# Performance work log

Hardware: AMD Instinct MI355X
Metric: run time of the kernel (lower is better)

The kernel has to match this reference:

```python
import jax, jax.numpy as jnp
import numpy as np

B, L, D = 16, 1024, 768   # batch, nodes per graph, embed_dim
H, C = 4, 256             # gat_heads, gat_hidden per head
E = 8192                  # directed edges per graph (2 per triple)
NEG_SLOPE = 0.2           # PyG GATConv default negative_slope


def setup_inputs() -> dict:
    key = jax.random.key(0)
    ks = jax.random.split(key, 8)
    s = 0.02
    return {
        "text_embeddings": jax.random.normal(ks[0], (B, L, D), jnp.float32),
        "edge_index": jax.random.randint(ks[1], (B, 2, E), 0, L, jnp.int32),
        "W_gat": jax.random.normal(ks[2], (H * C, D), jnp.float32) * s,   # GATConv.lin (bias=False)
        "att_src": jax.random.normal(ks[3], (H, C), jnp.float32) * s,
        "att_dst": jax.random.normal(ks[4], (H, C), jnp.float32) * s,
        "b_gat": jnp.zeros((H * C,), jnp.float32),                        # GATConv bias (concat=True)
        "W_out": jax.random.normal(ks[5], (D, H * C + D), jnp.float32) * s,
        "b_out": jnp.zeros((D,), jnp.float32),
    }


def _gat_one(x, edge_index, W_gat, att_src, att_dst, b_gat):
    """PyG-style GATConv on one graph. x: [N,D], edge_index: [2,E] (src->dst)."""
    N = x.shape[0]
    loops = jnp.arange(N, dtype=edge_index.dtype)          # add_self_loops=True (PyG default)
    src = jnp.concatenate([edge_index[0], loops])
    dst = jnp.concatenate([edge_index[1], loops])
    h = (x @ W_gat.T).reshape(N, H, C)                     # [N,H,C]
    a_s = jnp.einsum('nhc,hc->nh', h, att_src)             # [N,H]
    a_d = jnp.einsum('nhc,hc->nh', h, att_dst)
    e = jax.nn.leaky_relu(a_s[src] + a_d[dst], NEG_SLOPE)  # [E+N,H] per-edge logits
    m = jax.ops.segment_max(e, dst, num_segments=N)        # stable softmax over each dst neighborhood
    p = jnp.exp(e - m[dst])
    denom = jax.ops.segment_sum(p, dst, num_segments=N)
    alpha = p / (denom[dst] + 1e-16)                       # [E+N,H]
    out = jax.ops.segment_sum(alpha[:, :, None] * h[src], dst, num_segments=N)  # [N,H,C]
    return out.reshape(N, H * C) + b_gat


def reference(text_embeddings, edge_index, W_gat, att_src, att_dst, b_gat, W_out, b_out):
    x_gat = jax.vmap(_gat_one, in_axes=(0, 0, None, None, None, None))(
        text_embeddings, edge_index, W_gat, att_src, att_dst, b_gat)   # [B,L,H*C]
    fused = jnp.concatenate([text_embeddings, x_gat], axis=-1)          # [B,L,D+H*C]
    return fused @ W_out.T + b_out                                      # [B,L,D]
```

## Files before the change

### kernel.cpp

```cpp
#include <hip/hip_runtime.h>
#include <hip/hip_bf16.h>

#define B_ 16
#define L_ 1024
#define D_ 768
#define H_ 4
#define C_ 256
#define E_ 8192
#define ET_ (E_ + L_)
#define HC_ (H_ * C_)
#define F_ (D_ + HC_)
#define M_ (B_ * L_)
#define NEG_SLOPE 0.2f

typedef short bf16x8 __attribute__((ext_vector_type(8)));
typedef float f32x4 __attribute__((ext_vector_type(4)));
using bf16 = __hip_bfloat16;

struct bf16x4_s { bf16 x, y, z, w; };

__device__ __forceinline__ void async_copy16(const bf16* gsrc, bf16* ldst) {
  __builtin_amdgcn_global_load_lds(
      (const __attribute__((address_space(1))) unsigned int*)gsrc,
      (__attribute__((address_space(3))) unsigned int*)ldst, 16, 0, 0);
}

__global__ void cast_x_strided(const float* __restrict__ x, bf16* __restrict__ xf) {
  int idx = blockIdx.x * blockDim.x + threadIdx.x;
  if (idx >= M_ * (D_ / 8)) return;
  int row = idx / (D_ / 8);
  int c8 = idx - row * (D_ / 8);
  const float4* src = (const float4*)(x + (long)row * D_ + c8 * 8);
  float4 v0 = src[0], v1 = src[1];
  bf16 o[8];
  o[0] = __float2bfloat16(v0.x); o[1] = __float2bfloat16(v0.y);
  o[2] = __float2bfloat16(v0.z); o[3] = __float2bfloat16(v0.w);
  o[4] = __float2bfloat16(v1.x); o[5] = __float2bfloat16(v1.y);
  o[6] = __float2bfloat16(v1.z); o[7] = __float2bfloat16(v1.w);
  *(uint4*)(xf + (long)row * F_ + c8 * 8) = *(const uint4*)o;
}

__global__ void cast_two(const float4* __restrict__ a, bf16x4_s* __restrict__ oa, long na4,
                         const float4* __restrict__ bsrc, bf16x4_s* __restrict__ ob, long nb4) {
  long i = (long)blockIdx.x * blockDim.x + threadIdx.x;
  long stride = (long)gridDim.x * blockDim.x;
  for (; i < na4 + nb4; i += stride) {
    const float4 v = (i < na4) ? a[i] : bsrc[i - na4];
    bf16x4_s o;
    o.x = __float2bfloat16(v.x);
    o.y = __float2bfloat16(v.y);
    o.z = __float2bfloat16(v.z);
    o.w = __float2bfloat16(v.w);
    if (i < na4) oa[i] = o; else ob[i - na4] = o;
  }
}

#define BM 128
#define BN 128
#define BK 64

template <int OUT_BF16, int ATTN>
__global__ __launch_bounds__(256)
void gemm_nt_128(const bf16* __restrict__ A, int lda,
                 const bf16* __restrict__ Bm, int ldb,
                 void* __restrict__ Cm_, int ldc, int K,
                 const float* __restrict__ bias,
                 const float* __restrict__ att_s, const float* __restrict__ att_d,
                 float* __restrict__ a_sd)
{
  __shared__ __align__(16) bf16 As[BM * BK];
  __shared__ __align__(16) bf16 Bs[BN * BK];
  const int t = threadIdx.x;
  const int lane = t & 63;
  const int wave = t >> 6;
  const long m0 = (long)blockIdx.x * BM;
  const long n0 = (long)blockIdx.y * BN;
  const int wm = (wave >> 1) * 64;
  const int wn = (wave & 1) * 64;
  const int lrow = lane & 15;
  const int kq = lane >> 4;

  const int sr_base = wave * 32;
  const int sr_lane = lane >> 3;
  const int c8l = lane & 7;

  f32x4 acc[4][4] = {};

  for (int k0 = 0; k0 < K; k0 += BK) {
#pragma unroll
    for (int j = 0; j < 4; j++) {
      int r = sr_base + j * 8 + sr_lane;
      int col = k0 + ((c8l ^ (r & 7)) << 3);
      bf16* ldsA = As + (sr_base + j * 8) * BK;
      bf16* ldsB = Bs + (sr_base + j * 8) * BK;
      async_copy16(A + (m0 + r) * lda + col, ldsA);
      async_copy16(Bm + (n0 + r) * ldb + col, ldsB);
    }
    __syncthreads();
#pragma unroll
    for (int ks = 0; ks < BK; ks += 32) {
      bf16x8 af[4], bfr[4];
#pragma unroll
      for (int i = 0; i < 4; i++) {
        int ra = wm + i * 16 + lrow;
        int ca = ((ks >> 3) + kq) ^ (ra & 7);
        af[i] = *(const bf16x8*)(As + ra * BK + ca * 8);
        int rb = wn + i * 16 + lrow;
        int cb = ((ks >> 3) + kq) ^ (rb & 7);
        bfr[i] = *(const bf16x8*)(Bs + rb * BK + cb * 8);
      }
#pragma unroll
      for (int i = 0; i < 4; i++)
#pragma unroll
        for (int j = 0; j < 4; j++)
          acc[i][j] = __builtin_amdgcn_mfma_f32_16x16x32_bf16(af[i], bfr[j], acc[i][j], 0, 0, 0);
    }
    __syncthreads();
  }

#pragma unroll
  for (int i = 0; i < 4; i++) {
    long rbase = m0 + wm + i * 16 + (lane >> 4) * 4;
#pragma unroll
    for (int j = 0; j < 4; j++) {
      long col = n0 + wn + j * 16 + (lane & 15);
      float bv = bias ? bias[col] : 0.f;
#pragma unroll
      for (int r = 0; r < 4; r++) {
        long idx = (rbase + r) * ldc + col;
        float v = acc[i][j][r] + bv;
        if (OUT_BF16) ((bf16*)Cm_)[idx] = __float2bfloat16(v);
        else          ((float*)Cm_)[idx] = v;
      }
    }
  }

  if (ATTN) {
    float as_c[4], ad_c[4];
#pragma unroll
    for (int j = 0; j < 4; j++) {
      int col = (int)(n0 + wn + j * 16 + (lane & 15));
      as_c[j] = att_s[col];
      ad_c[j] = att_d[col];
    }
    const int head = (int)((n0 + wn) >> 8);
#pragma unroll
    for (int i = 0; i < 4; i++) {
#pragma unroll
      for (int r = 0; r < 4; r++) {
        float ps = 0.f, pd = 0.f;
#pragma unroll
        for (int j = 0; j < 4; j++) {
          float v = acc[i][j][r];
          ps += v * as_c[j];
          pd += v * ad_c[j];
        }
#pragma unroll
        for (int off = 1; off < 16; off <<= 1) {
          ps += __shfl_xor(ps, off);
          pd += __shfl_xor(pd, off);
        }
        if ((lane & 15) == 0) {
          long row = m0 + wm + i * 16 + (lane >> 4) * 4 + r;
          atomicAdd(a_sd + row * 8 + head, ps);
          atomicAdd(a_sd + row * 8 + 4 + head, pd);
        }
      }
    }
  }
}

__global__ void deg_count(const int* __restrict__ ei, int* __restrict__ deg) {
  int idx = blockIdx.x * blockDim.x + threadIdx.x;
  if (idx >= B_ * ET_) return;
  int b = idx / ET_, e = idx - b * ET_;
  int dst = (e < E_) ? ei[(long)b * 2 * E_ + E_ + e] : (e - E_);
  atomicAdd(&deg[b * L_ + dst], 1);
}

__global__ __launch_bounds__(1024)
void scan_offsets(const int* __restrict__ deg, int* __restrict__ offs,
                  int* __restrict__ cursor) {
  __shared__ int sh[1024];
  int b = blockIdx.x, t = threadIdx.x;
  int v = deg[b * L_ + t];
  sh[t] = v;
  __syncthreads();
  for (int d = 1; d < 1024; d <<= 1) {
    int x = (t >= d) ? sh[t - d] : 0;
    __syncthreads();
    sh[t] += x;
    __syncthreads();
  }
  int excl = sh[t] - v;
  offs[b * L_ + t] = excl;
  cursor[b * L_ + t] = excl;
}

__global__ void csr_fill(const int* __restrict__ ei, int* __restrict__ cursor,
                         int* __restrict__ csr_src) {
  int idx = blockIdx.x * blockDim.x + threadIdx.x;
  if (idx >= B_ * ET_) return;
  int b = idx / ET_, e = idx - b * ET_;
  int src, dst;
  if (e < E_) {
    src = ei[(long)b * 2 * E_ + e];
    dst = ei[(long)b * 2 * E_ + E_ + e];
  } else {
    src = dst = e - E_;
  }
  int slot = atomicAdd(&cursor[b * L_ + dst], 1);
  csr_src[(long)b * ET_ + slot] = src;
}

__device__ inline float lrelu(float v) { return v > 0.f ? v : NEG_SLOPE * v; }

__device__ __forceinline__ float sel4(float a0, float a1, float a2, float a3, int h) {
  float lo = (h & 1) ? a1 : a0;
  float hi = (h & 1) ? a3 : a2;
  return (h & 2) ? hi : lo;
}

__device__ __forceinline__ void fma8(float* acc, float a, uint4 u) {
#pragma unroll
  for (int k = 0; k < 4; k++) {
    unsigned w = ((const unsigned*)&u)[k];
    float lo = __uint_as_float(w << 16);
    float hi = __uint_as_float(w & 0xffff0000u);
    acc[2 * k]     += a * lo;
    acc[2 * k + 1] += a * hi;
  }
}

__global__ __launch_bounds__(256)
void gat_aggregate(const int* __restrict__ offs, const int* __restrict__ deg_a,
                   const int* __restrict__ csr_src,
                   const float* __restrict__ a_sd,
                   const bf16* __restrict__ h, bf16* __restrict__ xg, int ldx)
{
  const int bd = blockIdx.x * 4 + (threadIdx.x >> 6);
  const int b = bd >> 10;
  const int lane = threadIdx.x & 63;
  const int deg = deg_a[bd];
  const int* list = csr_src + (long)b * ET_ + offs[bd];
  const float4 ad = *(const float4*)(a_sd + (long)bd * 8 + 4);
  const int myhead = lane >> 4;
  const bf16* hbase = h + (long)b * L_ * HC_ + lane * 16;

  float acc16[16];
#pragma unroll
  for (int k = 0; k < 16; k++) acc16[k] = 0.f;

  if (deg <= 64) {
    int s_lane = 0;
    float4 e4 = {-INFINITY, -INFINITY, -INFINITY, -INFINITY};
    if (lane < deg) {
      s_lane = list[lane];
      const float4 as4 = *(const float4*)(a_sd + ((long)b * L_ + s_lane) * 8);
      e4.x = lrelu(as4.x + ad.x);
      e4.y = lrelu(as4.y + ad.y);
      e4.z = lrelu(as4.z + ad.z);
      e4.w = lrelu(as4.w + ad.w);
    }
    float4 mx = e4;
#pragma unroll
    for (int off = 32; off; off >>= 1) {
      mx.x = fmaxf(mx.x, __shfl_xor(mx.x, off));
      mx.y = fmaxf(mx.y, __shfl_xor(mx.y, off));
      mx.z = fmaxf(mx.z, __shfl_xor(mx.z, off));
      mx.w = fmaxf(mx.w, __shfl_xor(mx.w, off));
    }
    float4 p = {0.f, 0.f, 0.f, 0.f};
    if (lane < deg) {
      p.x = __expf(e4.x - mx.x);
      p.y = __expf(e4.y - mx.y);
      p.z = __expf(e4.z - mx.z);
      p.w = __expf(e4.w - mx.w);
    }
    float4 sm = p;
#pragma unroll
    for (int off = 32; off; off >>= 1) {
      sm.x += __shfl_xor(sm.x, off);
      sm.y += __shfl_xor(sm.y, off);
      sm.z += __shfl_xor(sm.z, off);
      sm.w += __shfl_xor(sm.w, off);
    }
    float4 alpha;
    alpha.x = p.x / (sm.x + 1e-16f);
    alpha.y = p.y / (sm.y + 1e-16f);
    alpha.z = p.z / (sm.z + 1e-16f);
    alpha.w = p.w / (sm.w + 1e-16f);

#pragma unroll 2
    for (int e = 0; e < deg; e++) {
      int se = __shfl(s_lane, e);
      float a0 = __shfl(alpha.x, e);
      float a1 = __shfl(alpha.y, e);
      float a2 = __shfl(alpha.z, e);
      float a3 = __shfl(alpha.w, e);
      float a = sel4(a0, a1, a2, a3, myhead);
      const bf16* hp = hbase + (long)se * HC_;
      uint4 u0 = *(const uint4*)hp;
      uint4 u1 = *(const uint4*)(hp + 8);
      fma8(acc16, a, u0);
      fma8(acc16 + 8, a, u1);
    }
  } else {
    float4 mx = {-INFINITY, -INFINITY, -INFINITY, -INFINITY};
    for (int i = lane; i < deg; i += 64) {
      int s = list[i];
      const float4 as4 = *(const float4*)(a_sd + ((long)b * L_ + s) * 8);
      mx.x = fmaxf(mx.x, lrelu(as4.x + ad.x));
      mx.y = fmaxf(mx.y, lrelu(as4.y + ad.y));
      mx.z = fmaxf(mx.z, lrelu(as4.z + ad.z));
      mx.w = fmaxf(mx.w, lrelu(as4.w + ad.w));
    }
#pragma unroll
    for (int off = 32; off; off >>= 1) {
      mx.x = fmaxf(mx.x, __shfl_xor(mx.x, off));
      mx.y = fmaxf(mx.y, __shfl_xor(mx.y, off));
      mx.z = fmaxf(mx.z, __shfl_xor(mx.z, off));
      mx.w = fmaxf(mx.w, __shfl_xor(mx.w, off));
    }
    float4 sm = {0.f, 0.f, 0.f, 0.f};
    for (int i = lane; i < deg; i += 64) {
      int s = list[i];
      const float4 as4 = *(const float4*)(a_sd + ((long)b * L_ + s) * 8);
      sm.x += __expf(lrelu(as4.x + ad.x) - mx.x);
      sm.y += __expf(lrelu(as4.y + ad.y) - mx.y);
      sm.z += __expf(lrelu(as4.z + ad.z) - mx.z);
      sm.w += __expf(lrelu(as4.w + ad.w) - mx.w);
    }
#pragma unroll
    for (int off = 32; off; off >>= 1) {
      sm.x += __shfl_xor(sm.x, off);
      sm.y += __shfl_xor(sm.y, off);
      sm.z += __shfl_xor(sm.z, off);
      sm.w += __shfl_xor(sm.w, off);
    }
    float4 rden;
    rden.x = 1.f / (sm.x + 1e-16f);
    rden.y = 1.f / (sm.y + 1e-16f);
    rden.z = 1.f / (sm.z + 1e-16f);
    rden.w = 1.f / (sm.w + 1e-16f);
    for (int e = 0; e < deg; e++) {
      int se = list[e];
      const float4 as4 = *(const float4*)(a_sd + ((long)b * L_ + se) * 8);
      float a0 = __expf(lrelu(as4.x + ad.x) - mx.x) * rden.x;
      float a1 = __expf(lrelu(as4.y + ad.y) - mx.y) * rden.y;
      float a2 = __expf(lrelu(as4.z + ad.z) - mx.z) * rden.z;
      float a3 = __expf(lrelu(as4.w + ad.w) - mx.w) * rden.w;
      float a = sel4(a0, a1, a2, a3, myhead);
      const bf16* hp = hbase + (long)se * HC_;
      uint4 u0 = *(const uint4*)hp;
      uint4 u1 = *(const uint4*)(hp + 8);
      fma8(acc16, a, u0);
      fma8(acc16 + 8, a, u1);
    }
  }

  bf16 ov[16];
#pragma unroll
  for (int k = 0; k < 16; k++) ov[k] = __float2bfloat16(acc16[k]);
  bf16* op = xg + (long)bd * ldx + lane * 16;
  *(uint4*)op = *(const uint4*)ov;
  *(uint4*)(op + 8) = *(const uint4*)(ov + 8);
}

__global__ void cout_kernel(const float* __restrict__ W_out, const float* __restrict__ b_gat,
                            const float* __restrict__ b_out, float* __restrict__ cout)
{
  int o = blockIdx.x * blockDim.x + threadIdx.x;
  if (o >= D_) return;
  float s = b_out[o];
  const float* wrow = W_out + (long)o * F_ + D_;
  for (int j = 0; j < HC_; j++) s += b_gat[j] * wrow[j];
  cout[o] = s;
}

extern "C" void kernel_launch(void* const* d_in, const int* in_sizes, int n_in,
                              void* d_out, int out_size, void* d_ws, size_t ws_size,
                              hipStream_t stream) {
  const float* x     = (const float*)d_in[0];
  const int*   ei    = (const int*)d_in[1];
  const float* Wg    = (const float*)d_in[2];
  const float* att_s = (const float*)d_in[3];
  const float* att_d = (const float*)d_in[4];
  const float* bgat  = (const float*)d_in[5];
  const float* Wout  = (const float*)d_in[6];
  const float* bout  = (const float*)d_in[7];
  float* out = (float*)d_out;

  char* ws = (char*)d_ws;
  size_t off = 0;
  auto alloc = [&](size_t bytes) {
    void* p = ws + off;
    off = (off + bytes + 255) & ~(size_t)255;
    return p;
  };
  bf16* xf      = (bf16*)alloc((size_t)M_ * F_ * 2);
  bf16* wg_bf   = (bf16*)alloc((size_t)HC_ * D_ * 2);
  bf16* wout_bf = (bf16*)alloc((size_t)D_ * F_ * 2);
  bf16* h_bf    = (bf16*)alloc((size_t)M_ * HC_ * 2);
  float* a_sd   = (float*)alloc((size_t)M_ * 8 * 4);
  int* deg      = (int*)alloc((size_t)M_ * 4);
  int* offs     = (int*)alloc((size_t)M_ * 4);
  int* cursor   = (int*)alloc((size_t)M_ * 4);
  int* csr_src  = (int*)alloc((size_t)B_ * ET_ * 4);
  float* cout   = (float*)alloc((size_t)D_ * 4);

  {
    int nchunk = M_ * (D_ / 8);
    cast_x_strided<<<dim3((nchunk + 255) / 256), dim3(256), 0, stream>>>(x, xf);
    long na4 = (long)HC_ * D_ / 4, nb4 = (long)D_ * F_ / 4;
    cast_two<<<dim3((int)((na4 + nb4 + 255) / 256)), dim3(256), 0, stream>>>(
        (const float4*)Wg, (bf16x4_s*)wg_bf, na4,
        (const float4*)Wout, (bf16x4_s*)wout_bf, nb4);
  }

  hipMemsetAsync(a_sd, 0, (size_t)M_ * 8 * 4 + (size_t)M_ * 4, stream);
  {
    int nedge = B_ * ET_;
    deg_count<<<dim3((nedge + 255) / 256), dim3(256), 0, stream>>>(ei, deg);
    scan_offsets<<<dim3(B_), dim3(1024), 0, stream>>>(deg, offs, cursor);
    csr_fill<<<dim3((nedge + 255) / 256), dim3(256), 0, stream>>>(ei, cursor, csr_src);
  }

  gemm_nt_128<1, 1><<<dim3(M_ / BM, HC_ / BN), dim3(256), 0, stream>>>(
      xf, F_, wg_bf, D_, h_bf, HC_, D_, nullptr, att_s, att_d, a_sd);

  gat_aggregate<<<dim3(M_ / 4), dim3(256), 0, stream>>>(offs, deg, csr_src, a_sd,
                                                        h_bf, xf + D_, F_);

  cout_kernel<<<dim3(3), dim3(256), 0, stream>>>(Wout, bgat, bout, cout);

  gemm_nt_128<0, 0><<<dim3(M_ / BM, D_ / BN), dim3(256), 0, stream>>>(
      xf, F_, wout_bf, F_, out, D_, F_, cout, nullptr, nullptr, nullptr);
}
```

Baseline: 319.7 us.

## Fuse prep kernels, fold attention into weights, switch GEMM to 32x32 MFMA

Several ideas land together. The attention vectors are folded into the GAT weight (W_gat^T·att) so the per-node logits come from a dot product on x in a fused prep kernel. That prep kernel also casts x, casts the weights and builds the CSR in shared memory, which replaces the separate memset, degree, scan, fill and cast launches and the atomic epilogue in the GEMM. The GEMM switches from 16x16x32 to 32x32x16 bf16 MFMA with 2x2 accumulator tiles. The folded logits are computed in fp32 from fp32 x rather than from bf16 h, which slightly changes numerics, and the CSR build now runs on only 16 blocks, which could serialize.

Measured after the change: 312.6 us. 1.02x faster.

```diff
diff --git a/kernel.cpp b/kernel.cpp
--- a/kernel.cpp
+++ b/kernel.cpp
@@ -14,7 +14,7 @@
 #define NEG_SLOPE 0.2f
 
 typedef short bf16x8 __attribute__((ext_vector_type(8)));
-typedef float f32x4 __attribute__((ext_vector_type(4)));
+typedef float f32x16 __attribute__((ext_vector_type(16)));
 using bf16 = __hip_bfloat16;
 
 struct bf16x4_s { bf16 x, y, z, w; };
@@ -25,33 +25,131 @@
       (__attribute__((address_space(3))) unsigned int*)ldst, 16, 0, 0);
 }
 
-__global__ void cast_x_strided(const float* __restrict__ x, bf16* __restrict__ xf) {
-  int idx = blockIdx.x * blockDim.x + threadIdx.x;
-  if (idx >= M_ * (D_ / 8)) return;
-  int row = idx / (D_ / 8);
-  int c8 = idx - row * (D_ / 8);
-  const float4* src = (const float4*)(x + (long)row * D_ + c8 * 8);
-  float4 v0 = src[0], v1 = src[1];
-  bf16 o[8];
-  o[0] = __float2bfloat16(v0.x); o[1] = __float2bfloat16(v0.y);
-  o[2] = __float2bfloat16(v0.z); o[3] = __float2bfloat16(v0.w);
-  o[4] = __float2bfloat16(v1.x); o[5] = __float2bfloat16(v1.y);
-  o[6] = __float2bfloat16(v1.z); o[7] = __float2bfloat16(v1.w);
-  *(uint4*)(xf + (long)row * F_ + c8 * 8) = *(const uint4*)o;
-}
-
-__global__ void cast_two(const float4* __restrict__ a, bf16x4_s* __restrict__ oa, long na4,
-                         const float4* __restrict__ bsrc, bf16x4_s* __restrict__ ob, long nb4) {
-  long i = (long)blockIdx.x * blockDim.x + threadIdx.x;
-  long stride = (long)gridDim.x * blockDim.x;
-  for (; i < na4 + nb4; i += stride) {
-    const float4 v = (i < na4) ? a[i] : bsrc[i - na4];
-    bf16x4_s o;
-    o.x = __float2bfloat16(v.x);
-    o.y = __float2bfloat16(v.y);
-    o.z = __float2bfloat16(v.z);
-    o.w = __float2bfloat16(v.w);
-    if (i < na4) oa[i] = o; else ob[i - na4] = o;
+__global__ __launch_bounds__(256)
+void precompute(const float* __restrict__ Wg,
+                const float* __restrict__ att_s, const float* __restrict__ att_d,
+                const float* __restrict__ Wout, const float* __restrict__ bgat,
+                const float* __restrict__ bout,
+                float* __restrict__ wsd, float* __restrict__ cout)
+{
+  int blk = blockIdx.x, t = threadIdx.x;
+  if (blk < 24) {
+    int h8 = blk / 3;
+    int k = (blk % 3) * 256 + t;
+    const float* att = (h8 < 4) ? (att_s + h8 * C_) : (att_d + (h8 - 4) * C_);
+    int head = h8 & 3;
+    const float* wbase = Wg + (long)head * C_ * D_ + k;
+    float acc = 0.f;
+    for (int c = 0; c < C_; c++) acc += att[c] * wbase[(long)c * D_];
+    wsd[h8 * D_ + k] = acc;
+  } else {
+    int o = (blk - 24) * 256 + t;
+    if (o < D_) {
+      float s = bout[o];
+      const float* wrow = Wout + (long)o * F_ + D_;
+      for (int j = 0; j < HC_; j++) s += bgat[j] * wrow[j];
+      cout[o] = s;
+    }
+  }
+}
+
+#define NB_CSR 16
+#define NB_X (M_ / 4)
+#define NB_W 2112
+
+__global__ __launch_bounds__(256)
+void prep(const float* __restrict__ x, const int* __restrict__ ei,
+          const float* __restrict__ Wg, const float* __restrict__ Wout,
+          const float* __restrict__ wsd,
+          bf16* __restrict__ xf, bf16* __restrict__ wg_bf, bf16* __restrict__ wout_bf,
+          float* __restrict__ a_sd, int* __restrict__ deg_g, int* __restrict__ offs_g,
+          int* __restrict__ csr_src)
+{
+  __shared__ int s_deg[L_];
+  __shared__ int s_cur[L_];
+  __shared__ int s_part[256];
+  const int blk = blockIdx.x;
+  const int t = threadIdx.x;
+
+  if (blk < NB_CSR) {
+    const int b = blk;
+    const int* srcp = ei + (long)b * 2 * E_;
+    const int* dstp = srcp + E_;
+    for (int i = t; i < L_; i += 256) s_deg[i] = 0;
+    __syncthreads();
+    for (int e = t; e < ET_; e += 256) {
+      int dst = (e < E_) ? dstp[e] : (e - E_);
+      atomicAdd(&s_deg[dst], 1);
+    }
+    __syncthreads();
+    int d0 = s_deg[t*4], d1 = s_deg[t*4+1], d2 = s_deg[t*4+2], d3 = s_deg[t*4+3];
+    int tsum = d0 + d1 + d2 + d3;
+    s_part[t] = tsum;
+    __syncthreads();
+    for (int o = 1; o < 256; o <<= 1) {
+      int v = (t >= o) ? s_part[t - o] : 0;
+      __syncthreads();
+      s_part[t] += v;
+      __syncthreads();
+    }
+    int run = s_part[t] - tsum;
+    int o0 = run, o1 = o0 + d0, o2 = o1 + d1, o3 = o2 + d2;
+    s_cur[t*4] = o0; s_cur[t*4+1] = o1; s_cur[t*4+2] = o2; s_cur[t*4+3] = o3;
+    int gb = b * L_ + t * 4;
+    offs_g[gb] = o0; offs_g[gb+1] = o1; offs_g[gb+2] = o2; offs_g[gb+3] = o3;
+    deg_g[gb] = d0; deg_g[gb+1] = d1; deg_g[gb+2] = d2; deg_g[gb+3] = d3;
+    __syncthreads();
+    int* csr_b = csr_src + (long)b * ET_;
+    for (int e = t; e < ET_; e += 256) {
+      int src = (e < E_) ? srcp[e] : (e - E_);
+      int dst = (e < E_) ? dstp[e] : (e - E_);
+      int slot = atomicAdd(&s_cur[dst], 1);
+      csr_b[slot] = src;
+    }
+  } else if (blk < NB_CSR + NB_X) {
+    int row = (blk - NB_CSR) * 4 + (t >> 6);
+    int lane = t & 63;
+    const float4* xr = (const float4*)(x + (long)row * D_);
+    float acc8[8];
+#pragma unroll
+    for (int h = 0; h < 8; h++) acc8[h] = 0.f;
+#pragma unroll
+    for (int q = 0; q < 3; q++) {
+      float4 v = xr[lane + 64 * q];
+      bf16 o4[4] = { __float2bfloat16(v.x), __float2bfloat16(v.y),
+                     __float2bfloat16(v.z), __float2bfloat16(v.w) };
+      *(uint2*)(xf + (long)row * F_ + 4 * (lane + 64 * q)) = *(const uint2*)o4;
+#pragma unroll
+      for (int h = 0; h < 8; h++) {
+        float4 w = ((const float4*)(wsd + h * D_))[lane + 64 * q];
+        acc8[h] += v.x * w.x + v.y * w.y + v.z * w.z + v.w * w.w;
+      }
+    }
+#pragma unroll
+    for (int o = 32; o; o >>= 1)
+#pragma unroll
+      for (int h = 0; h < 8; h++) acc8[h] += __shfl_xor(acc8[h], o);
+    if (lane == 0) {
+      float4 s4 = {acc8[0], acc8[1], acc8[2], acc8[3]};
+      float4 dd4 = {acc8[4], acc8[5], acc8[6], acc8[7]};
+      *(float4*)(a_sd + (long)row * 8) = s4;
+      *(float4*)(a_sd + (long)row * 8 + 4) = dd4;
+    }
+  } else {
+    long na4 = (long)HC_ * D_ / 4;
+    long nb4 = (long)D_ * F_ / 4;
+    long i0 = (long)(blk - NB_CSR - NB_X) * 256 + t;
+    long stride = (long)NB_W * 256;
+    for (long i = i0; i < na4 + nb4; i += stride) {
+      const float4 v = (i < na4) ? ((const float4*)Wg)[i] : ((const float4*)Wout)[i - na4];
+      bf16x4_s o;
+      o.x = __float2bfloat16(v.x);
+      o.y = __float2bfloat16(v.y);
+      o.z = __float2bfloat16(v.z);
+      o.w = __float2bfloat16(v.w);
+      if (i < na4) ((bf16x4_s*)wg_bf)[i] = o;
+      else         ((bf16x4_s*)wout_bf)[i - na4] = o;
+    }
   }
 }
 
@@ -59,14 +157,12 @@
 #define BN 128
 #define BK 64
 
-template <int OUT_BF16, int ATTN>
+template <int OUT_BF16>
 __global__ __launch_bounds__(256)
 void gemm_nt_128(const bf16* __restrict__ A, int lda,
                  const bf16* __restrict__ Bm, int ldb,
                  void* __restrict__ Cm_, int ldc, int K,
-                 const float* __restrict__ bias,
-                 const float* __restrict__ att_s, const float* __restrict__ att_d,
-                 float* __restrict__ a_sd)
+                 const float* __restrict__ bias)
 {
   __shared__ __align__(16) bf16 As[BM * BK];
   __shared__ __align__(16) bf16 Bs[BN * BK];
@@ -77,14 +173,14 @@
   const long n0 = (long)blockIdx.y * BN;
   const int wm = (wave >> 1) * 64;
   const int wn = (wave & 1) * 64;
-  const int lrow = lane & 15;
-  const int kq = lane >> 4;
+  const int lrow = lane & 31;
+  const int kg = lane >> 5;
 
   const int sr_base = wave * 32;
   const int sr_lane = lane >> 3;
   const int c8l = lane & 7;
 
-  f32x4 acc[4][4] = {};
+  f32x16 acc[2][2] = {};
 
   for (int k0 = 0; k0 < K; k0 += BK) {
 #pragma unroll
@@ -98,119 +194,41 @@
     }
     __syncthreads();
 #pragma unroll
-    for (int ks = 0; ks < BK; ks += 32) {
-      bf16x8 af[4], bfr[4];
-#pragma unroll
-      for (int i = 0; i < 4; i++) {
-        int ra = wm + i * 16 + lrow;
-        int ca = ((ks >> 3) + kq) ^ (ra & 7);
+    for (int ks = 0; ks < BK; ks += 16) {
+      bf16x8 af[2], bfr[2];
+#pragma unroll
+      for (int i = 0; i < 2; i++) {
+        int ra = wm + i * 32 + lrow;
+        int ca = ((ks >> 3) + kg) ^ (ra & 7);
         af[i] = *(const bf16x8*)(As + ra * BK + ca * 8);
-        int rb = wn + i * 16 + lrow;
-        int cb = ((ks >> 3) + kq) ^ (rb & 7);
+        int rb = wn + i * 32 + lrow;
+        int cb = ((ks >> 3) + kg) ^ (rb & 7);
         bfr[i] = *(const bf16x8*)(Bs + rb * BK + cb * 8);
       }
 #pragma unroll
-      for (int i = 0; i < 4; i++)
-#pragma unroll
-        for (int j = 0; j < 4; j++)
-          acc[i][j] = __builtin_amdgcn_mfma_f32_16x16x32_bf16(af[i], bfr[j], acc[i][j], 0, 0, 0);
-    }
-    __syncthreads();
-  }
-
-#pragma unroll
-  for (int i = 0; i < 4; i++) {
-    long rbase = m0 + wm + i * 16 + (lane >> 4) * 4;
-#pragma unroll
-    for (int j = 0; j < 4; j++) {
-      long col = n0 + wn + j * 16 + (lane & 15);
+      for (int i = 0; i < 2; i++)
+#pragma unroll
+        for (int j = 0; j < 2; j++)
+          acc[i][j] = __builtin_amdgcn_mfma_f32_32x32x16_bf16(af[i], bfr[j], acc[i][j], 0, 0, 0);
+    }
+    __syncthreads();
+  }
+
+#pragma unroll
+  for (int i = 0; i < 2; i++) {
+#pragma unroll
+    for (int j = 0; j < 2; j++) {
+      long col = n0 + wn + j * 32 + lrow;
       float bv = bias ? bias[col] : 0.f;
 #pragma unroll
-      for (int r = 0; r < 4; r++) {
-        long idx = (rbase + r) * ldc + col;
-        float v = acc[i][j][r] + bv;
-        if (OUT_BF16) ((bf16*)Cm_)[idx] = __float2bfloat16(v);
-        else          ((float*)Cm_)[idx] = v;
+      for (int reg = 0; reg < 16; reg++) {
+        long row = m0 + wm + i * 32 + (reg & 3) + 8 * (reg >> 2) + 4 * kg;
+        float v = acc[i][j][reg] + bv;
+        if (OUT_BF16) ((bf16*)Cm_)[row * ldc + col] = __float2bfloat16(v);
+        else          ((float*)Cm_)[row * ldc + col] = v;
       }
     }
   }
-
-  if (ATTN) {
-    float as_c[4], ad_c[4];
-#pragma unroll
-    for (int j = 0; j < 4; j++) {
-      int col = (int)(n0 + wn + j * 16 + (lane & 15));
-      as_c[j] = att_s[col];
-      ad_c[j] = att_d[col];
-    }
-    const int head = (int)((n0 + wn) >> 8);
-#pragma unroll
-    for (int i = 0; i < 4; i++) {
-#pragma unroll
-      for (int r = 0; r < 4; r++) {
-        float ps = 0.f, pd = 0.f;
-#pragma unroll
-        for (int j = 0; j < 4; j++) {
-          float v = acc[i][j][r];
-          ps += v * as_c[j];
-          pd += v * ad_c[j];
-        }
-#pragma unroll
-        for (int off = 1; off < 16; off <<= 1) {
-          ps += __shfl_xor(ps, off);
-          pd += __shfl_xor(pd, off);
-        }
-        if ((lane & 15) == 0) {
-          long row = m0 + wm + i * 16 + (lane >> 4) * 4 + r;
-          atomicAdd(a_sd + row * 8 + head, ps);
-          atomicAdd(a_sd + row * 8 + 4 + head, pd);
-        }
-      }
-    }
-  }
-}
-
-__global__ void deg_count(const int* __restrict__ ei, int* __restrict__ deg) {
-  int idx = blockIdx.x * blockDim.x + threadIdx.x;
-  if (idx >= B_ * ET_) return;
-  int b = idx / ET_, e = idx - b * ET_;
-  int dst = (e < E_) ? ei[(long)b * 2 * E_ + E_ + e] : (e - E_);
-  atomicAdd(&deg[b * L_ + dst], 1);
-}
-
-__global__ __launch_bounds__(1024)
-void scan_offsets(const int* __restrict__ deg, int* __restrict__ offs,
-                  int* __restrict__ cursor) {
-  __shared__ int sh[1024];
-  int b = blockIdx.x, t = threadIdx.x;
-  int v = deg[b * L_ + t];
-  sh[t] = v;
-  __syncthreads();
-  for (int d = 1; d < 1024; d <<= 1) {
-    int x = (t >= d) ? sh[t - d] : 0;
-    __syncthreads();
-    sh[t] += x;
-    __syncthreads();
-  }
-  int excl = sh[t] - v;
-  offs[b * L_ + t] = excl;
-  cursor[b * L_ + t] = excl;
-}
-
-__global__ void csr_fill(const int* __restrict__ ei, int* __restrict__ cursor,
-                         int* __restrict__ csr_src) {
-  int idx = blockIdx.x * blockDim.x + threadIdx.x;
-  if (idx >= B_ * ET_) return;
-  int b = idx / ET_, e = idx - b * ET_;
-  int src, dst;
-  if (e < E_) {
-    src = ei[(long)b * 2 * E_ + e];
-    dst = ei[(long)b * 2 * E_ + E_ + e];
-  } else {
-    src = dst = e - E_;
-  }
-  int slot = atomicAdd(&cursor[b * L_ + dst], 1);
-  csr_src[(long)b * ET_ + slot] = src;
 }
 
 __device__ inline float lrelu(float v) { return v > 0.f ? v : NEG_SLOPE * v; }
@@ -367,17 +385,6 @@
   *(uint4*)(op + 8) = *(const uint4*)(ov + 8);
 }
 
-__global__ void cout_kernel(const float* __restrict__ W_out, const float* __restrict__ b_gat,
-                            const float* __restrict__ b_out, float* __restrict__ cout)
-{
-  int o = blockIdx.x * blockDim.x + threadIdx.x;
-  if (o >= D_) return;
-  float s = b_out[o];
-  const float* wrow = W_out + (long)o * F_ + D_;
-  for (int j = 0; j < HC_; j++) s += b_gat[j] * wrow[j];
-  cout[o] = s;
-}
-
 extern "C" void kernel_launch(void* const* d_in, const int* in_sizes, int n_in,
                               void* d_out, int out_size, void* d_ws, size_t ws_size,
                               hipStream_t stream) {
@@ -405,35 +412,22 @@
   float* a_sd   = (float*)alloc((size_t)M_ * 8 * 4);
   int* deg      = (int*)alloc((size_t)M_ * 4);
   int* offs     = (int*)alloc((size_t)M_ * 4);
-  int* cursor   = (int*)alloc((size_t)M_ * 4);
   int* csr_src  = (int*)alloc((size_t)B_ * ET_ * 4);
   float* cout   = (float*)alloc((size_t)D_ * 4);
-
-  {
-    int nchunk = M_ * (D_ / 8);
-    cast_x_strided<<<dim3((nchunk + 255) / 256), dim3(256), 0, stream>>>(x, xf);
-    long na4 = (long)HC_ * D_ / 4, nb4 = (long)D_ * F_ / 4;
-    cast_two<<<dim3((int)((na4 + nb4 + 255) / 256)), dim3(256), 0, stream>>>(
-        (const float4*)Wg, (bf16x4_s*)wg_bf, na4,
-        (const float4*)Wout, (bf16x4_s*)wout_bf, nb4);
-  }
-
-  hipMemsetAsync(a_sd, 0, (size_t)M_ * 8 * 4 + (size_t)M_ * 4, stream);
-  {
-    int nedge = B_ * ET_;
-    deg_count<<<dim3((nedge + 255) / 256), dim3(256), 0, stream>>>(ei, deg);
-    scan_offsets<<<dim3(B_), dim3(1024), 0, stream>>>(deg, offs, cursor);
-    csr_fill<<<dim3((nedge + 255) / 256), dim3(256), 0, stream>>>(ei, cursor, csr_src);
-  }
-
-  gemm_nt_128<1, 1><<<dim3(M_ / BM, HC_ / BN), dim3(256), 0, stream>>>(
-      xf, F_, wg_bf, D_, h_bf, HC_, D_, nullptr, att_s, att_d, a_sd);
+  float* wsd    = (float*)alloc((size_t)8 * D_ * 4);
+
+  precompute<<<dim3(27), dim3(256), 0, stream>>>(Wg, att_s, att_d, Wout, bgat, bout,
+                                                 wsd, cout);
+
+  prep<<<dim3(NB_CSR + NB_X + NB_W), dim3(256), 0, stream>>>(
+      x, ei, Wg, Wout, wsd, xf, wg_bf, wout_bf, a_sd, deg, offs, csr_src);
+
+  gemm_nt_128<1><<<dim3(M_ / BM, HC_ / BN), dim3(256), 0, stream>>>(
+      xf, F_, wg_bf, D_, h_bf, HC_, D_, nullptr);
 
   gat_aggregate<<<dim3(M_ / 4), dim3(256), 0, stream>>>(offs, deg, csr_src, a_sd,
                                                         h_bf, xf + D_, F_);
 
-  cout_kernel<<<dim3(3), dim3(256), 0, stream>>>(Wout, bgat, bout, cout);
-
-  gemm_nt_128<0, 0><<<dim3(M_ / BM, D_ / BN), dim3(256), 0, stream>>>(
-      xf, F_, wout_bf, F_, out, D_, F_, cout, nullptr, nullptr, nullptr);
-}
+  gemm_nt_128<0><<<dim3(M_ / BM, D_ / BN), dim3(256), 0, stream>>>(
+      xf, F_, wout_bf, F_, out, D_, F_, cout);
+}
```
